# Kernel tuning notes

Measured on AMD Instinct MI355X. Metric: run time of the kernel, lower is better.

Reference implementation:

```python
import jax, jax.numpy as jnp
import numpy as np

R_FRAC = 0.5  # r_token


def setup_inputs() -> dict:
    key = jax.random.key(0)
    B, T, C = 64, 577, 1024
    hidden_states = jax.random.normal(key, (B, T, C), dtype=jnp.float32)
    return {"hidden_states": hidden_states}


def _match_indices(x, r):
    # Bipartite soft matching (class_token=True, distill_token=False).
    metric = x / jnp.linalg.norm(x, axis=-1, keepdims=True)
    a, b = metric[:, ::2, :], metric[:, 1::2, :]  # [B, Ta, C], [B, Tb, C]
    scores = jnp.einsum('bic,bjc->bij', a, b)     # [B, Ta, Tb]
    scores = scores.at[:, 0, :].set(-jnp.inf)     # protect CLS token (even index 0)
    node_max = scores.max(axis=-1)                # best sim of each src to any dst
    node_idx = scores.argmax(axis=-1)             # matched dst for each src
    edge_idx = jnp.argsort(-node_max, axis=-1)    # descending by similarity
    unm_idx = jnp.sort(edge_idx[:, r:], axis=-1)  # unmerged src (sorted: keeps CLS first)
    src_idx = edge_idx[:, :r]                     # src tokens to merge
    dst_idx = jnp.take_along_axis(node_idx, src_idx, axis=-1)
    return unm_idx, src_idx, dst_idx


def _merge_sum(v, unm_idx, src_idx, dst_idx):
    # Gather unmerged + scatter-add merged src into dst, then concat.
    src, dst = v[:, ::2, :], v[:, 1::2, :]
    unm = jnp.take_along_axis(src, unm_idx[..., None], axis=1)
    srcg = jnp.take_along_axis(src, src_idx[..., None], axis=1)
    dst = jax.vmap(lambda d, i, s: d.at[i].add(s))(dst, dst_idx, srcg)
    return jnp.concatenate([unm, dst], axis=1)


def reference(hidden_states):
    x = hidden_states
    B, T, C = x.shape
    protected = 1  # class token
    r = min(int(R_FRAC * T), (T - protected) // 2)  # 288 for T=577
    unm_idx, src_idx, dst_idx = _match_indices(x, r)
    # merge_wavg with size=None -> size = ones
    size = jnp.ones((B, T, 1), dtype=x.dtype)
    xm = _merge_sum(x * size, unm_idx, src_idx, dst_idx)
    sm = _merge_sum(size, unm_idx, src_idx, dst_idx)
    return xm / sm  # [B, T - r, C]
```

## Files before the change

kernel.cpp:

```cpp
#include <hip/hip_runtime.h>
#include <math.h>


#define B_   64
#define T_   577
#define C_   1024
#define NA   289
#define NB   288
#define EPS_MARGIN 0.01f

#define RPAD 384
#define EXTRA_CAP 12

typedef __bf16 bf16x8 __attribute__((ext_vector_type(8)));
typedef float  floatx4 __attribute__((ext_vector_type(4)));
typedef unsigned long long u64;

#define ECNT_OFF   0
#define GRPWIN_OFF 98304
#define EXTRA_OFF  (GRPWIN_OFF + 1179648)
#define DST_OFF    (EXTRA_OFF + 2359296)

__device__ __forceinline__ u64 shfl_xor_u64(u64 v, int msk) {
  unsigned int lo = (unsigned int)v, hi = (unsigned int)(v >> 32);
  lo = __shfl_xor(lo, msk, 64);
  hi = __shfl_xor(hi, msk, 64);
  return ((u64)hi << 32) | (u64)lo;
}
__device__ __forceinline__ double shfl_xor_f64(double v, int msk) {
  u64 u = __double_as_longlong(v);
  return __longlong_as_double((long long)shfl_xor_u64(u, msk));
}

__device__ __forceinline__ unsigned int fkey(float s) {
  unsigned int fb = __float_as_uint(s);
  return (fb & 0x80000000u) ? ~fb : (fb | 0x80000000u);
}
__device__ __forceinline__ float keyf(unsigned int k) {
  return (k & 0x80000000u) ? __uint_as_float(k ^ 0x80000000u) : __uint_as_float(~k);
}
__device__ __forceinline__ u64 packsc(float s, int col) {
  return ((u64)fkey(s) << 32) | (u64)(0xFFFFFFFFu - (unsigned int)col);
}
__device__ __forceinline__ int pcol(u64 p) {
  return (int)(0xFFFFFFFFu - (unsigned int)(p & 0xFFFFFFFFull));
}
__device__ __forceinline__ float pscore(u64 p) { return keyf((unsigned int)(p >> 32)); }

__device__ __forceinline__ unsigned int pk_bf16_trunc(unsigned int e1, unsigned int e0) {
  return __builtin_amdgcn_perm(e1, e0, 0x07060302u);
}

__device__ __forceinline__ void load16f(const float* x, size_t off, float* v) {
  const float4* p = (const float4*)(x + off);
  float4 a = p[0], b = p[1], c = p[2], d = p[3];
  v[0]=a.x; v[1]=a.y; v[2]=a.z; v[3]=a.w;
  v[4]=b.x; v[5]=b.y; v[6]=b.z; v[7]=b.w;
  v[8]=c.x; v[9]=c.y; v[10]=c.z; v[11]=c.w;
  v[12]=d.x; v[13]=d.y; v[14]=d.z; v[15]=d.w;
}


#define LOADC(S, KCC) do {                                                    \
  _Pragma("unroll")                                                           \
  for (int e_ = 0; e_ < 6; ++e_) {                                            \
    const uint4* p_ = (const uint4*)(eptr[e_] + (KCC) * 64);                  \
    S[e_][0] = p_[0]; S[e_][1] = p_[1];                                       \
  }                                                                           \
} while (0)

#define STAGEC(S, BUFP) do {                                                  \
  unsigned char* sb_ = (BUFP);                                                \
  _Pragma("unroll")                                                           \
  for (int e_ = 0; e_ < 6; ++e_) {                                            \
    uint4 lo_ = S[e_][0], hi_ = S[e_][1];                                     \
    uint4 o_;                                                                 \
    o_.x = pk_bf16_trunc(lo_.y, lo_.x);                                       \
    o_.y = pk_bf16_trunc(lo_.w, lo_.z);                                       \
    o_.z = pk_bf16_trunc(hi_.y, hi_.x);                                       \
    o_.w = pk_bf16_trunc(hi_.w, hi_.z);                                       \
    *(uint4*)(sb_ + eoff[e_]) = o_;                                           \
    if (e_ >= 3) {                                                            \
      float f0_ = __uint_as_float(lo_.x), f1_ = __uint_as_float(lo_.y);       \
      float f2_ = __uint_as_float(lo_.z), f3_ = __uint_as_float(lo_.w);       \
      float f4_ = __uint_as_float(hi_.x), f5_ = __uint_as_float(hi_.y);       \
      float f6_ = __uint_as_float(hi_.z), f7_ = __uint_as_float(hi_.w);       \
      ssp[e_-3] += f0_*f0_ + f1_*f1_ + f2_*f2_ + f3_*f3_                      \
                 + f4_*f4_ + f5_*f5_ + f6_*f6_ + f7_*f7_;                     \
    }                                                                         \
  }                                                                           \
} while (0)

#define MFMAC(BUFP) do {                                                      \
  const unsigned char* buf_ = (BUFP);                                         \
  _Pragma("unroll")                                                           \
  for (int s_ = 0; s_ < 2; ++s_) {                                            \
    int slot_ = (s_ * 4 + q) ^ sw;                                            \
    bf16x8 af_[3], bg_[3];                                                    \
    _Pragma("unroll")                                                         \
    for (int ii_ = 0; ii_ < 3; ++ii_)                                         \
      af_[ii_] = *(const bf16x8*)(buf_ + ((ib + ii_) * 16 + m) * 128 + slot_ * 16); \
    _Pragma("unroll")                                                         \
    for (int jj_ = 0; jj_ < 3; ++jj_)                                         \
      bg_[jj_] = *(const bf16x8*)(buf_ + 12288 + ((jb + jj_) * 16 + m) * 128 + slot_ * 16); \
    _Pragma("unroll")                                                         \
    for (int ii_ = 0; ii_ < 3; ++ii_)                                         \
      _Pragma("unroll")                                                       \
      for (int jj_ = 0; jj_ < 3; ++jj_)                                       \
        acc[ii_][jj_] = __builtin_amdgcn_mfma_f32_16x16x32_bf16(af_[ii_], bg_[jj_], acc[ii_][jj_], 0, 0, 0); \
  }                                                                           \
} while (0)

__global__ __launch_bounds__(256, 2) void k_scores(const float* __restrict__ x,
                                                   u64* __restrict__ grpwin,
                                                   unsigned int* __restrict__ ecnt,
                                                   u64* __restrict__ extras) {
  __shared__ unsigned char smem[2][24576];
  __shared__ float sumsq[96];
  int tid = threadIdx.x;
  int b  = blockIdx.x;
  int rt = blockIdx.y;
  int ct = blockIdx.z;
  int wv = tid >> 6, lane = tid & 63;
  int m = lane & 15, q = lane >> 4;
  int sw = m & 7;

  if (tid < 96) sumsq[tid] = 0.f;

  const float* eptr[6];
  int eoff[6];
#pragma unroll
  for (int e = 0; e < 6; ++e) {
    int v = tid + 256 * e;
    int isB = v >= 768;
    int w = isB ? v - 768 : v;
    int row = w >> 3, slot = w & 7;
    int gk = slot ^ (row & 7);
    int tok;
    if (isB) tok = 2 * (ct * 96 + row) + 1;
    else { tok = 2 * (rt * 96 + row); if (tok > 576) tok = 576; }
    eptr[e] = x + (size_t)(b * T_ + tok) * C_ + gk * 8;
    eoff[e] = (isB ? 12288 : 0) + row * 128 + slot * 16;
  }

  float ssp[3] = {0.f, 0.f, 0.f};
  uint4 SA[6][2], SB[6][2];

  floatx4 acc[3][3];
#pragma unroll
  for (int ii = 0; ii < 3; ++ii)
#pragma unroll
    for (int jj = 0; jj < 3; ++jj) acc[ii][jj] = (floatx4){0,0,0,0};

  const int ib = (wv >> 1) * 3;
  const int jb = (wv & 1) * 3;

  LOADC(SA, 0);
  LOADC(SB, 1);
  __builtin_amdgcn_sched_barrier(0);
  STAGEC(SA, smem[0]);
  __syncthreads();

  for (int kc2 = 0; kc2 < 14; kc2 += 2) {
    LOADC(SA, kc2 + 2);
    __builtin_amdgcn_sched_barrier(0);
    STAGEC(SB, smem[1]);
    MFMAC(smem[0]);
    __syncthreads();
    LOADC(SB, kc2 + 3);
    __builtin_amdgcn_sched_barrier(0);
    STAGEC(SA, smem[0]);
    MFMAC(smem[1]);
    __syncthreads();
  }
  STAGEC(SB, smem[1]);
  MFMAC(smem[0]);
  __syncthreads();
  MFMAC(smem[1]);

#pragma unroll
  for (int e = 3; e < 6; ++e) {
    int w = tid + 256 * e - 768;
    atomicAdd(&sumsq[w >> 3], ssp[e-3]);
  }
  __syncthreads();

  float rn[3];
#pragma unroll
  for (int jj = 0; jj < 3; ++jj) rn[jj] = rsqrtf(sumsq[(jb + jj) * 16 + m]);

  int g = ct * 2 + (wv & 1);
#pragma unroll
  for (int ii = 0; ii < 3; ++ii) {
#pragma unroll
    for (int r = 0; r < 4; ++r) {
      u64 pj[3];
#pragma unroll
      for (int jj = 0; jj < 3; ++jj) {
        float s = acc[ii][jj][r] * rn[jj];
        pj[jj] = packsc(s, ct * 96 + (jb + jj) * 16 + m);
      }
      u64 pk = pj[0];
      if (pj[1] > pk) pk = pj[1];
      if (pj[2] > pk) pk = pj[2];
#pragma unroll
      for (int d = 1; d < 16; d <<= 1) {
        u64 o = shfl_xor_u64(pk, d);
        if (o > pk) pk = o;
      }
      int grow = rt * 96 + (ib + ii) * 16 + q * 4 + r;
      float thr = pscore(pk) - EPS_MARGIN;
      size_t rbase = (size_t)b * RPAD + grow;
#pragma unroll
      for (int jj = 0; jj < 3; ++jj) {
        if (pj[jj] != pk && pscore(pj[jj]) >= thr) {
          unsigned int idx = atomicAdd(&ecnt[rbase], 1u);
          if (idx < EXTRA_CAP) extras[rbase * EXTRA_CAP + idx] = pj[jj];
        }
      }
      if (m == 0) grpwin[rbase * 6 + g] = pk;
    }
  }
}

__global__ __launch_bounds__(256) void k_recheck(const float* __restrict__ x,
                                                 const u64* __restrict__ grpwin,
                                                 const unsigned int* __restrict__ ecnt,
                                                 const u64* __restrict__ extras,
                                                 int* __restrict__ dst) {
  int wid = threadIdx.x >> 6, lane = threadIdx.x & 63;
  int gw = blockIdx.x * 4 + wid;
  int b = gw / NB, i = gw - b * NB + 1;
  size_t rbase = (size_t)b * RPAD + i;

  u64 v = (lane < 6) ? grpwin[rbase * 6 + lane] : 0ull;
#pragma unroll
  for (int d = 1; d < 8; d <<= 1) {
    u64 o = shfl_xor_u64(v, d);
    if (o > v) v = o;
  }
  {
    unsigned int lo = (unsigned int)v, hi = (unsigned int)(v >> 32);
    lo = __shfl(lo, 0, 64); hi = __shfl(hi, 0, 64);
    v = ((u64)hi << 32) | lo;
  }
  float thr = pscore(v) - EPS_MARGIN;

  u64 cand[14]; int nc = 0;
#pragma unroll
  for (int t = 0; t < 6; ++t) {
    u64 w = grpwin[rbase * 6 + t];
    if (pscore(w) >= thr && nc < 14) cand[nc++] = w;
  }
  unsigned int ec = ecnt[rbase]; if (ec > EXTRA_CAP) ec = EXTRA_CAP;
  for (unsigned int t = 0; t < ec; ++t) {
    u64 w = extras[rbase * EXTRA_CAP + t];
    if (pscore(w) >= thr && nc < 14) cand[nc++] = w;
  }

  int best;
  if (nc <= 1) {
    best = pcol(v);
  } else {
    float av[16];
    load16f(x, (size_t)(b * T_ + 2 * i) * C_ + lane * 16, av);
    double bs = -1e300; int bc = 1 << 30;
    for (int c = 0; c < nc; ++c) {
      int col = pcol(cand[c]);
      float bv[16];
      load16f(x, (size_t)(b * T_ + 2 * col + 1) * C_ + lane * 16, bv);
      double dot = 0.0, nsq = 0.0;
#pragma unroll
      for (int t = 0; t < 16; ++t) {
        dot += (double)av[t] * (double)bv[t];
        nsq += (double)bv[t] * (double)bv[t];
      }
#pragma unroll
      for (int d = 32; d >= 1; d >>= 1) {
        dot += shfl_xor_f64(dot, d);
        nsq += shfl_xor_f64(nsq, d);
      }
      double s = dot / sqrt(nsq);
      if (s > bs || (s == bs && col < bc)) { bs = s; bc = col; }
    }
    best = bc;
  }
  if (lane == 0) dst[b * NA + i] = best;
}

__global__ __launch_bounds__(256) void k_merge(const float* __restrict__ x,
                                               const int* __restrict__ dst,
                                               float* __restrict__ out) {
  __shared__ int dstv[NA];
  __shared__ unsigned short lists[4][292];
  __shared__ int cnts[4];
  int b = blockIdx.y, tid = threadIdx.x;
  int orow_base = blockIdx.x * 4;

  for (int i = tid; i < NA; i += 256) dstv[i] = (i >= 1) ? dst[b * NA + i] : -1;
  if (tid < 4) cnts[tid] = 0;
  __syncthreads();

  for (int i = 1 + tid; i <= 288; i += 256) {
    int d = dstv[i];
#pragma unroll
    for (int w4 = 0; w4 < 4; ++w4) {
      int orow_w = orow_base + w4;
      if (orow_w >= 1 && orow_w < NA && d == orow_w - 1) {
        int idx = atomicAdd(&cnts[w4], 1);
        lists[w4][idx] = (unsigned short)i;
      }
    }
  }
  __syncthreads();

  int wv = tid >> 6, lane = tid & 63;
  int orow = orow_base + wv;
  if (orow >= NA) return;

  const size_t xb = (size_t)b * T_ * C_;
  int c0 = lane * 16;
  float acc[16];
  float inv = 1.0f;

  if (orow == 0) {
    load16f(x, xb + c0, acc);
  } else {
    int j = orow - 1;
    load16f(x, xb + (size_t)(2 * j + 1) * C_ + c0, acc);
    int cnt = cnts[wv];
    for (int e = 0; e < cnt; ++e) {
      int i = lists[wv][e];
      float tv[16];
      load16f(x, xb + (size_t)(2 * i) * C_ + c0, tv);
#pragma unroll
      for (int t = 0; t < 16; ++t) acc[t] += tv[t];
    }
    inv = 1.0f / (float)(cnt + 1);
  }

  float4* op = (float4*)(out + ((size_t)b * NA + orow) * C_ + c0);
  op[0] = make_float4(acc[0]*inv,  acc[1]*inv,  acc[2]*inv,  acc[3]*inv);
  op[1] = make_float4(acc[4]*inv,  acc[5]*inv,  acc[6]*inv,  acc[7]*inv);
  op[2] = make_float4(acc[8]*inv,  acc[9]*inv,  acc[10]*inv, acc[11]*inv);
  op[3] = make_float4(acc[12]*inv, acc[13]*inv, acc[14]*inv, acc[15]*inv);
}

extern "C" void kernel_launch(void* const* d_in, const int* in_sizes, int n_in,
                              void* d_out, int out_size, void* d_ws, size_t ws_size,
                              hipStream_t stream) {
  const float* x = (const float*)d_in[0];
  float* out     = (float*)d_out;
  char* ws = (char*)d_ws;
  unsigned int* ecnt = (unsigned int*)(ws + ECNT_OFF);
  u64* grpwin        = (u64*)(ws + GRPWIN_OFF);
  u64* extras        = (u64*)(ws + EXTRA_OFF);
  int* dst           = (int*)(ws + DST_OFF);

  hipMemsetAsync(ecnt, 0, (size_t)B_ * RPAD * sizeof(unsigned int), stream);
  k_scores <<<dim3(B_, 4, 3), 256, 0, stream>>>(x, grpwin, ecnt, extras);
  k_recheck<<<B_ * NB / 4, 256, 0, stream>>>(x, grpwin, ecnt, extras, dst);
  k_merge  <<<dim3((NA + 3) / 4, B_), 256, 0, stream>>>(x, dst, out);
}
```

Before: 319.4 us.

## Pre-normalize tokens to bf16 in a prep kernel and stage via direct global-to-LDS loads

Adds a k_prep kernel that L2-normalizes every token and writes a swizzled bf16 copy into the output buffer as scratch. k_scores then streams this half-size bf16 data straight into LDS with global_load_lds, dropping the register round trip, the fp32-to-bf16 conversion and the sum-of-squares reduction. Scores no longer need rescaling by row norms. The cost is an extra full pass over the input plus a write and re-read of the bf16 copy, and it relies on d_out being large enough and not yet needed.

Result: slower. 345.5 us (+8.2%).

```diff
diff --git a/kernel.cpp b/kernel.cpp
--- a/kernel.cpp
+++ b/kernel.cpp
@@ -60,35 +60,52 @@
   v[12]=d.x; v[13]=d.y; v[14]=d.z; v[15]=d.w;
 }
 
-
-#define LOADC(S, KCC) do {                                                    \
+__global__ __launch_bounds__(256) void k_prep(const float* __restrict__ x,
+                                              unsigned int* __restrict__ y) {
+  int wv = threadIdx.x >> 6, lane = threadIdx.x & 63;
+  int token = blockIdx.x * 4 + wv;
+  int t = token % T_;
+  int r8 = (t >> 1) & 7;
+
+  float v[16];
+  load16f(x, (size_t)token * C_ + lane * 16, v);
+  float ss = 0.f;
+#pragma unroll
+  for (int i = 0; i < 16; ++i) ss += v[i] * v[i];
+#pragma unroll
+  for (int d = 1; d < 64; d <<= 1) ss += __shfl_xor(ss, d, 64);
+  float rn = rsqrtf(ss);
+#pragma unroll
+  for (int i = 0; i < 16; ++i) v[i] *= rn;
+
+  uint4 g0, g1;
+  g0.x = pk_bf16_trunc(__float_as_uint(v[1]),  __float_as_uint(v[0]));
+  g0.y = pk_bf16_trunc(__float_as_uint(v[3]),  __float_as_uint(v[2]));
+  g0.z = pk_bf16_trunc(__float_as_uint(v[5]),  __float_as_uint(v[4]));
+  g0.w = pk_bf16_trunc(__float_as_uint(v[7]),  __float_as_uint(v[6]));
+  g1.x = pk_bf16_trunc(__float_as_uint(v[9]),  __float_as_uint(v[8]));
+  g1.y = pk_bf16_trunc(__float_as_uint(v[11]), __float_as_uint(v[10]));
+  g1.z = pk_bf16_trunc(__float_as_uint(v[13]), __float_as_uint(v[12]));
+  g1.w = pk_bf16_trunc(__float_as_uint(v[15]), __float_as_uint(v[14]));
+
+  int ga = 2 * lane, gb = 2 * lane + 1;
+  int da = (ga & ~7) | ((ga & 7) ^ r8);
+  int db = (gb & ~7) | ((gb & 7) ^ r8);
+  uint4* yb = (uint4*)((char*)y + (size_t)token * 2048);
+  yb[da] = g0;
+  yb[db] = g1;
+}
+
+
+#define GLOADLDS16(GP, LP)                                                    \
+  __builtin_amdgcn_global_load_lds(                                           \
+      (const __attribute__((address_space(1))) void*)(GP),                    \
+      (__attribute__((address_space(3))) void*)(LP), 16, 0, 0)
+
+#define STAGE(CUR, KC) do {                                                   \
   _Pragma("unroll")                                                           \
-  for (int e_ = 0; e_ < 6; ++e_) {                                            \
-    const uint4* p_ = (const uint4*)(eptr[e_] + (KCC) * 64);                  \
-    S[e_][0] = p_[0]; S[e_][1] = p_[1];                                       \
-  }                                                                           \
-} while (0)
-
-#define STAGEC(S, BUFP) do {                                                  \
-  unsigned char* sb_ = (BUFP);                                                \
-  _Pragma("unroll")                                                           \
-  for (int e_ = 0; e_ < 6; ++e_) {                                            \
-    uint4 lo_ = S[e_][0], hi_ = S[e_][1];                                     \
-    uint4 o_;                                                                 \
-    o_.x = pk_bf16_trunc(lo_.y, lo_.x);                                       \
-    o_.y = pk_bf16_trunc(lo_.w, lo_.z);                                       \
-    o_.z = pk_bf16_trunc(hi_.y, hi_.x);                                       \
-    o_.w = pk_bf16_trunc(hi_.w, hi_.z);                                       \
-    *(uint4*)(sb_ + eoff[e_]) = o_;                                           \
-    if (e_ >= 3) {                                                            \
-      float f0_ = __uint_as_float(lo_.x), f1_ = __uint_as_float(lo_.y);       \
-      float f2_ = __uint_as_float(lo_.z), f3_ = __uint_as_float(lo_.w);       \
-      float f4_ = __uint_as_float(hi_.x), f5_ = __uint_as_float(hi_.y);       \
-      float f6_ = __uint_as_float(hi_.z), f7_ = __uint_as_float(hi_.w);       \
-      ssp[e_-3] += f0_*f0_ + f1_*f1_ + f2_*f2_ + f3_*f3_                      \
-                 + f4_*f4_ + f5_*f5_ + f6_*f6_ + f7_*f7_;                     \
-    }                                                                         \
-  }                                                                           \
+  for (int e_ = 0; e_ < 6; ++e_)                                              \
+    GLOADLDS16(src[e_] + (KC) * 128, smem[CUR] + ldsoff[e_]);                 \
 } while (0)
 
 #define MFMAC(BUFP) do {                                                      \
@@ -111,12 +128,11 @@
   }                                                                           \
 } while (0)
 
-__global__ __launch_bounds__(256, 2) void k_scores(const float* __restrict__ x,
+__global__ __launch_bounds__(256, 2) void k_scores(const unsigned int* __restrict__ y,
                                                    u64* __restrict__ grpwin,
                                                    unsigned int* __restrict__ ecnt,
                                                    u64* __restrict__ extras) {
   __shared__ unsigned char smem[2][24576];
-  __shared__ float sumsq[96];
   int tid = threadIdx.x;
   int b  = blockIdx.x;
   int rt = blockIdx.y;
@@ -125,69 +141,41 @@
   int m = lane & 15, q = lane >> 4;
   int sw = m & 7;
 
-  if (tid < 96) sumsq[tid] = 0.f;
-
-  const float* eptr[6];
-  int eoff[6];
+  const char* src[6];
+  int ldsoff[6];
 #pragma unroll
   for (int e = 0; e < 6; ++e) {
-    int v = tid + 256 * e;
-    int isB = v >= 768;
-    int w = isB ? v - 768 : v;
-    int row = w >> 3, slot = w & 7;
-    int gk = slot ^ (row & 7);
+    int L = ((wv * 6 + e) * 64 + lane) * 16;
+    int row = L >> 7;
+    int sl  = (L >> 4) & 7;
+    int isB = row >= 96;
+    int r2  = isB ? row - 96 : row;
     int tok;
-    if (isB) tok = 2 * (ct * 96 + row) + 1;
-    else { tok = 2 * (rt * 96 + row); if (tok > 576) tok = 576; }
-    eptr[e] = x + (size_t)(b * T_ + tok) * C_ + gk * 8;
-    eoff[e] = (isB ? 12288 : 0) + row * 128 + slot * 16;
-  }
-
-  float ssp[3] = {0.f, 0.f, 0.f};
-  uint4 SA[6][2], SB[6][2];
+    if (isB) tok = 2 * (ct * 96 + r2) + 1;
+    else { tok = 2 * (rt * 96 + r2); if (tok > 576) tok = 576; }
+    src[e] = (const char*)y + (size_t)(b * T_ + tok) * 2048 + sl * 16;
+    ldsoff[e] = (wv * 6 + e) * 1024;
+  }
 
   floatx4 acc[3][3];
 #pragma unroll
   for (int ii = 0; ii < 3; ++ii)
 #pragma unroll
-    for (int jj = 0; jj < 3; ++jj) acc[ii][jj] = (floatx4){0,0,0,0};
+    for (int jj = 0; jj < 3; ++jj) acc[ii][jj] = (floatx4){0, 0, 0, 0};
 
   const int ib = (wv >> 1) * 3;
   const int jb = (wv & 1) * 3;
 
-  LOADC(SA, 0);
-  LOADC(SB, 1);
-  __builtin_amdgcn_sched_barrier(0);
-  STAGEC(SA, smem[0]);
+  STAGE(0, 0);
   __syncthreads();
-
-  for (int kc2 = 0; kc2 < 14; kc2 += 2) {
-    LOADC(SA, kc2 + 2);
-    __builtin_amdgcn_sched_barrier(0);
-    STAGEC(SB, smem[1]);
-    MFMAC(smem[0]);
+  int cur = 0;
+  for (int kc = 0; kc < 15; ++kc) {
+    STAGE(cur ^ 1, kc + 1);
+    MFMAC(smem[cur]);
     __syncthreads();
-    LOADC(SB, kc2 + 3);
-    __builtin_amdgcn_sched_barrier(0);
-    STAGEC(SA, smem[0]);
-    MFMAC(smem[1]);
-    __syncthreads();
-  }
-  STAGEC(SB, smem[1]);
-  MFMAC(smem[0]);
-  __syncthreads();
-  MFMAC(smem[1]);
-
-#pragma unroll
-  for (int e = 3; e < 6; ++e) {
-    int w = tid + 256 * e - 768;
-    atomicAdd(&sumsq[w >> 3], ssp[e-3]);
-  }
-  __syncthreads();
-
-  float rn[3];
-#pragma unroll
-  for (int jj = 0; jj < 3; ++jj) rn[jj] = rsqrtf(sumsq[(jb + jj) * 16 + m]);
+    cur ^= 1;
+  }
+  MFMAC(smem[cur]);
 
   int g = ct * 2 + (wv & 1);
 #pragma unroll
@@ -197,7 +185,7 @@
       u64 pj[3];
 #pragma unroll
       for (int jj = 0; jj < 3; ++jj) {
-        float s = acc[ii][jj][r] * rn[jj];
+        float s = acc[ii][jj][r];
         pj[jj] = packsc(s, ct * 96 + (jb + jj) * 16 + m);
       }
       u64 pk = pj[0];
@@ -357,8 +345,11 @@
   u64* extras        = (u64*)(ws + EXTRA_OFF);
   int* dst           = (int*)(ws + DST_OFF);
 
+  unsigned int* y = (unsigned int*)d_out;
+
   hipMemsetAsync(ecnt, 0, (size_t)B_ * RPAD * sizeof(unsigned int), stream);
-  k_scores <<<dim3(B_, 4, 3), 256, 0, stream>>>(x, grpwin, ecnt, extras);
+  k_prep   <<<(B_ * T_) / 4, 256, 0, stream>>>(x, y);
+  k_scores <<<dim3(B_, 4, 3), 256, 0, stream>>>(y, grpwin, ecnt, extras);
   k_recheck<<<B_ * NB / 4, 256, 0, stream>>>(x, grpwin, ecnt, extras, dst);
   k_merge  <<<dim3((NA + 3) / 4, B_), 256, 0, stream>>>(x, dst, out);
 }
```
